# Performance work log

Hardware: AMD Instinct MI355X
Metric: run time of the kernel (lower is better)

## Reference

```python
import jax, jax.numpy as jnp
import numpy as np

B, S, D_IN, D_ATT = 8, 2048, 512, 512

def setup_inputs() -> dict:
    key = jax.random.key(0)
    ks = jax.random.split(key, 7)
    sc = 1.0 / np.sqrt(D_IN)
    return {
        "x": jax.random.normal(ks[0], (B, S, D_IN), dtype=jnp.float32),
        "Wq": jax.random.uniform(ks[1], (D_IN, D_ATT), jnp.float32, -sc, sc),
        "bq": jax.random.uniform(ks[2], (D_ATT,), jnp.float32, -sc, sc),
        "Wk": jax.random.uniform(ks[3], (D_IN, D_ATT), jnp.float32, -sc, sc),
        "bk": jax.random.uniform(ks[4], (D_ATT,), jnp.float32, -sc, sc),
        "Wv": jax.random.uniform(ks[5], (D_IN, D_ATT), jnp.float32, -sc, sc),
        "bv": jax.random.uniform(ks[6], (D_ATT,), jnp.float32, -sc, sc),
    }

def reference(x, Wq, bq, Wk, bk, Wv, bv):
    # Linear projections: [B, S, D_att]
    q = jnp.einsum("bsd,de->bse", x, Wq) + bq
    k = jnp.einsum("bsd,de->bse", x, Wk) + bk
    v = jnp.einsum("bsd,de->bse", x, Wv) + bv
    # Full scores matrix [B, S, S]; note: NO 1/sqrt(d) scaling in original.
    scores = jnp.einsum("bqe,bke->bqk", q, k)
    attn = jax.nn.softmax(scores, axis=-1)
    return jnp.einsum("bqk,bke->bqe", attn, v)
```

## Files before the change

### kernel.cpp

```cpp
#include <hip/hip_runtime.h>
#include <cstdint>
#include <cstddef>


#define SEQ 2048
#define DIM 512
#define NB 8
#define BSZ (NB * SEQ)
#define KT 64
#define NT (SEQ / KT)

typedef __attribute__((ext_vector_type(8))) _Float16 half8;
typedef __attribute__((ext_vector_type(4))) _Float16 half4;
typedef __attribute__((ext_vector_type(2))) __fp16 fp16x2;
typedef __attribute__((ext_vector_type(4))) float f32x4;
typedef __attribute__((ext_vector_type(16))) float f32x16;

__device__ __forceinline__ unsigned short f2h(float f) {
  _Float16 h = (_Float16)f;
  return __builtin_bit_cast(unsigned short, h);
}
__device__ __forceinline__ half8 ld_frag(const unsigned short* p) {
  return *(const half8*)(const void*)p;
}
__device__ __forceinline__ void gl_lds16(const unsigned short* g, unsigned short* l) {
  __builtin_amdgcn_global_load_lds(
      (__attribute__((address_space(1))) void*)g,
      (__attribute__((address_space(3))) void*)l, 16, 0, 0);
}
__device__ __forceinline__ void bar_vm0() {
  asm volatile("s_waitcnt vmcnt(0)\ns_barrier" ::: "memory");
}
__device__ __forceinline__ void bar_lgkm() {
  asm volatile("s_waitcnt lgkmcnt(0)\ns_barrier" ::: "memory");
}
__device__ __forceinline__ void bar_lgkm_vm0() {
  asm volatile("s_waitcnt lgkmcnt(0) vmcnt(0)\ns_barrier" ::: "memory");
}

__global__ __launch_bounds__(256) void cvt_x_kernel(
    const float* __restrict__ X, unsigned short* __restrict__ xh)
{
  size_t i0 = ((size_t)blockIdx.x * 256 + threadIdx.x) * 8;
  float4 a = *(const float4*)&X[i0];
  float4 b = *(const float4*)&X[i0 + 4];
  ushort4 o0; o0.x = f2h(a.x); o0.y = f2h(a.y); o0.z = f2h(a.z); o0.w = f2h(a.w);
  ushort4 o1; o1.x = f2h(b.x); o1.y = f2h(b.y); o1.z = f2h(b.z); o1.w = f2h(b.w);
  *(ushort4*)&xh[i0] = o0;
  *(ushort4*)&xh[i0 + 4] = o1;
}

__global__ __launch_bounds__(256) void cvt_w_kernel(
    const float* __restrict__ Wq, const float* __restrict__ Wk,
    const float* __restrict__ Wv, unsigned short* __restrict__ Wt)
{
  const int z = blockIdx.z;
  const float* W = (z == 0) ? Wq : (z == 1) ? Wk : Wv;
  unsigned short* out = Wt + (size_t)z * DIM * DIM;
  const int k0 = blockIdx.x * 64, n0 = blockIdx.y * 64;
  const int t = threadIdx.x;
  __shared__ unsigned short tl[64 * 72];
#pragma unroll
  for (int i = 0; i < 4; i++) {
    int f = t + 256 * i;
    int kr = f >> 4, c4 = (f & 15) * 4;
    float4 v = *(const float4*)&W[(size_t)(k0 + kr) * DIM + n0 + c4];
    tl[(c4 + 0) * 72 + kr] = f2h(v.x);
    tl[(c4 + 1) * 72 + kr] = f2h(v.y);
    tl[(c4 + 2) * 72 + kr] = f2h(v.z);
    tl[(c4 + 3) * 72 + kr] = f2h(v.w);
  }
  __syncthreads();
#pragma unroll
  for (int i = 0; i < 2; i++) {
    int f = t + 256 * i;
    int nr = f >> 3, k8 = (f & 7) * 8;
    *(uint4*)&out[(size_t)(n0 + nr) * DIM + k0 + k8] = *(const uint4*)&tl[nr * 72 + k8];
  }
}

__global__ __launch_bounds__(256) void proj_kernel(
    const unsigned short* __restrict__ xh, const unsigned short* __restrict__ Wt,
    const float* __restrict__ bq, const float* __restrict__ bk,
    const float* __restrict__ bv, unsigned short* __restrict__ outbase)
{
  const int z = blockIdx.z;
  const unsigned short* Wz = Wt + (size_t)z * DIM * DIM;
  const float* bias = (z == 0) ? bq : (z == 1) ? bk : bv;
  unsigned short* out = outbase + (size_t)z * BSZ * DIM;
  const int m0 = blockIdx.x * 128, n0 = blockIdx.y * 128;
  const int t = threadIdx.x, lane = t & 63, wave = t >> 6;
  const int wrow = (wave >> 1) * 64, wcol = (wave & 1) * 64;
  const int lr = lane & 15, lq = (lane >> 4) * 8;

  __shared__ unsigned short sm[128 * 132];
  unsigned short* As = sm;
  unsigned short* Bs = sm + 128 * 64;

  f32x4 acc[4][4];
  const f32x4 zero = {0.f, 0.f, 0.f, 0.f};
#pragma unroll
  for (int r = 0; r < 4; r++)
#pragma unroll
    for (int c = 0; c < 4; c++) acc[r][c] = zero;

  for (int k0 = 0; k0 < DIM; k0 += 64) {
    __syncthreads();
#pragma unroll
    for (int i = 0; i < 4; i++) {
      int f = t + 256 * i;
      int row = f >> 3, c8 = (f & 7) * 8;
      gl_lds16(&xh[(size_t)(m0 + row) * DIM + k0 + c8], &As[i * 2048 + wave * 512]);
      gl_lds16(&Wz[(size_t)(n0 + row) * DIM + k0 + c8], &Bs[i * 2048 + wave * 512]);
    }
    __syncthreads();
#pragma unroll
    for (int kk = 0; kk < 64; kk += 32) {
      half8 a[4], b[4];
#pragma unroll
      for (int r = 0; r < 4; r++) a[r] = ld_frag(&As[(wrow + 16 * r + lr) * 64 + kk + lq]);
#pragma unroll
      for (int c = 0; c < 4; c++) b[c] = ld_frag(&Bs[(wcol + 16 * c + lr) * 64 + kk + lq]);
#pragma unroll
      for (int r = 0; r < 4; r++)
#pragma unroll
        for (int c = 0; c < 4; c++)
          acc[r][c] = __builtin_amdgcn_mfma_f32_16x16x32_f16(a[r], b[c], acc[r][c], 0, 0, 0);
    }
  }
  __syncthreads();
#pragma unroll
  for (int c = 0; c < 4; c++) {
    float bb = bias[n0 + wcol + 16 * c + lr];
#pragma unroll
    for (int r = 0; r < 4; r++)
#pragma unroll
      for (int e = 0; e < 4; e++)
        sm[(wrow + 16 * r + (lane >> 4) * 4 + e) * 132 + wcol + 16 * c + lr] =
            f2h(acc[r][c][e] + bb);
  }
  __syncthreads();
#pragma unroll
  for (int i = 0; i < 8; i++) {
    int f = t + 256 * i;
    int row = f >> 4, c8 = (f & 15) * 8;
    *(uint4*)&out[(size_t)(m0 + row) * DIM + n0 + c8] = *(const uint4*)&sm[row * 132 + c8];
  }
}

__global__ __launch_bounds__(256) void vtrans_kernel(
    const unsigned short* __restrict__ vh, unsigned short* __restrict__ vt)
{
  const int b = blockIdx.z;
  const int s0 = blockIdx.x * 64, n0 = blockIdx.y * 64;
  const int t = threadIdx.x;
  __shared__ unsigned short tl[64 * 72];
#pragma unroll
  for (int i = 0; i < 2; i++) {
    int f = t + 256 * i;
    int sr = f >> 3, c8 = (f & 7) * 8;
    uint4 raw = *(const uint4*)&vh[((size_t)b * SEQ + s0 + sr) * DIM + n0 + c8];
    unsigned short u[8];
    *(uint4*)u = raw;
#pragma unroll
    for (int j = 0; j < 8; j++) tl[(c8 + j) * 72 + sr] = u[j];
  }
  __syncthreads();
#pragma unroll
  for (int i = 0; i < 2; i++) {
    int f = t + 256 * i;
    int nr = f >> 3, s8 = (f & 7) * 8;
    *(uint4*)&vt[((size_t)b * DIM + n0 + nr) * SEQ + s0 + s8] = *(const uint4*)&tl[nr * 72 + s8];
  }
}

#define PSTR 68
#define OSTR 516

__global__ __launch_bounds__(256, 1) void flash_kernel(
    const unsigned short* __restrict__ Qb, const unsigned short* __restrict__ Kb,
    const unsigned short* __restrict__ Vtb, float* __restrict__ Ob)
{
  const int zb = blockIdx.x & 7;
  const int q0 = (blockIdx.x >> 3) * 64;
  const unsigned short* Q = Qb + (size_t)zb * SEQ * DIM;
  const unsigned short* K = Kb + (size_t)zb * SEQ * DIM;
  const unsigned short* V = Vtb + (size_t)zb * DIM * SEQ;
  float* Out = Ob + (size_t)zb * SEQ * DIM;

  const int t = threadIdx.x, lane = t & 63, wave = t >> 6;
  const int l31 = lane & 31, hi = lane >> 5;
  const int kh = wave & 1, rh = wave >> 1;
  const int lr = lane & 15, lq4 = lane >> 4;
  const float L2E = 1.4426950408889634f;

  __shared__ unsigned short lds[70664];
  unsigned short* Qbuf = lds;
  unsigned short* Kbuf = lds + 32768;
  unsigned short* Pbuf = lds + 65536;
  float* mpart = (float*)(lds + 65536 + 64 * PSTR);
  float* lpart = mpart + 128;
  float* abuf = lpart + 128;
  float* lrun = abuf + 64;
  unsigned int* fbuf = (unsigned int*)(lrun + 64);

  if (t < 64) lrun[t] = 0.f;

  int koff[16];
#pragma unroll
  for (int i = 0; i < 16; i++) {
    int f = t + 256 * i;
    int row = f >> 6, c = f & 63;
    koff[i] = row * DIM + (c ^ (row & 7)) * 8;
  }

#pragma unroll
  for (int i = 0; i < 16; i++)
    gl_lds16(&Q[(size_t)q0 * DIM + koff[i]], &Qbuf[i * 2048 + wave * 512]);
#pragma unroll
  for (int i = 0; i < 16; i++)
    gl_lds16(&K[koff[i]], &Kbuf[i * 2048 + wave * 512]);

  f32x4 acc[32];
  const f32x4 zero = {0.f, 0.f, 0.f, 0.f};
#pragma unroll
  for (int ob = 0; ob < 32; ob++) acc[ob] = zero;
  float m_run = -__builtin_inff();

  const int keyrow = kh * 32 + l31, ksw = keyrow & 7;
  const int qrow = rh * 32 + l31, qsw = qrow & 7;
  const unsigned short* Kc = Kbuf + keyrow * 512;
  const unsigned short* Qc = Qbuf + qrow * 512;

  for (int kt = 0; kt < NT; kt++) {
    bar_vm0();

    const unsigned short* Vb = V + (size_t)(wave * 128 + lr) * SEQ + kt * KT + lq4 * 8;
    half8 vfA[8];
#pragma unroll
    for (int dc = 0; dc < 4; dc++)
#pragma unroll
      for (int ks = 0; ks < 2; ks++)
        vfA[dc * 2 + ks] = ld_frag(Vb + (size_t)dc * 16 * SEQ + ks * 32);

    f32x16 s0 = {0.f, 0.f, 0.f, 0.f, 0.f, 0.f, 0.f, 0.f,
                 0.f, 0.f, 0.f, 0.f, 0.f, 0.f, 0.f, 0.f};
    f32x16 s1 = s0;
    __builtin_amdgcn_s_setprio(1);
#pragma unroll
    for (int j = 0; j < 16; j++) {
      half8 kf0 = ld_frag(&Kc[((2 * j + hi) ^ ksw) << 3]);
      half8 qv0 = ld_frag(&Qc[((2 * j + hi) ^ qsw) << 3]);
      half8 kf1 = ld_frag(&Kc[((2 * (j + 16) + hi) ^ ksw) << 3]);
      half8 qv1 = ld_frag(&Qc[((2 * (j + 16) + hi) ^ qsw) << 3]);
      s0 = __builtin_amdgcn_mfma_f32_32x32x16_f16(kf0, qv0, s0, 0, 0, 0);
      s1 = __builtin_amdgcn_mfma_f32_32x32x16_f16(kf1, qv1, s1, 0, 0, 0);
    }
    __builtin_amdgcn_s_setprio(0);
    f32x16 sacc = s0 + s1;

    float mx = sacc[0];
#pragma unroll
    for (int i2 = 1; i2 < 16; i2++) mx = fmaxf(mx, sacc[i2]);
    mx = fmaxf(mx, __shfl_xor(mx, 32, 64));
    if (lane < 32) mpart[kh * 64 + rh * 32 + lane] = mx;
    bar_lgkm();

    if (kt + 1 < NT) {
      const unsigned short* Kt = K + (size_t)(kt + 1) * KT * DIM;
#pragma unroll
      for (int i = 0; i < 16; i++)
        gl_lds16(&Kt[koff[i]], &Kbuf[i * 2048 + wave * 512]);
    }
    half8 vfB[8];
#pragma unroll
    for (int dc = 0; dc < 4; dc++)
#pragma unroll
      for (int ks = 0; ks < 2; ks++)
        vfB[dc * 2 + ks] = ld_frag(Vb + (size_t)(dc + 4) * 16 * SEQ + ks * 32);

    float mo = mpart[(kh ^ 1) * 64 + rh * 32 + l31];
    float mxc = fmaxf(mx, mo);
    bool keep = (mxc - m_run <= 8.0f);
    float mnew = keep ? m_run : mxc;
    float alpha = keep ? 1.0f : exp2f((m_run - mnew) * L2E);
    m_run = mnew;
    if (kh == 0 && lane < 32) abuf[rh * 32 + lane] = alpha;
    unsigned long long ball = __ballot(keep);
    if (lane == 0) fbuf[wave] = (ball == ~0ull) ? 1u : 0u;

    float psum = 0.f;
#pragma unroll
    for (int w2 = 0; w2 < 4; w2++) {
      float p0 = exp2f((sacc[4 * w2 + 0] - mnew) * L2E);
      float p1 = exp2f((sacc[4 * w2 + 1] - mnew) * L2E);
      float p2 = exp2f((sacc[4 * w2 + 2] - mnew) * L2E);
      float p3 = exp2f((sacc[4 * w2 + 3] - mnew) * L2E);
      psum += (p0 + p1) + (p2 + p3);
      fp16x2 pa = __builtin_amdgcn_cvt_pkrtz(p0, p1);
      fp16x2 pb = __builtin_amdgcn_cvt_pkrtz(p2, p3);
      unsigned long long both =
          ((unsigned long long)__builtin_bit_cast(unsigned int, pb) << 32) |
          __builtin_bit_cast(unsigned int, pa);
      *(unsigned long long*)&Pbuf[qrow * PSTR + kh * 32 + w2 * 8 + 4 * hi] = both;
    }
    psum += __shfl_xor(psum, 32, 64);
    if (lane < 32) lpart[kh * 64 + rh * 32 + lane] = psum;
    bar_lgkm();
    if (kh == 0 && lane < 32) {
      int r = rh * 32 + lane;
      lrun[r] = alpha * lrun[r] + lpart[r] + lpart[64 + r];
    }

    if (!(fbuf[0] & fbuf[1] & fbuf[2] & fbuf[3])) {
#pragma unroll
      for (int rg = 0; rg < 4; rg++)
#pragma unroll
        for (int e = 0; e < 4; e++) {
          float a = abuf[rg * 16 + lq4 * 4 + e];
#pragma unroll
          for (int dc = 0; dc < 8; dc++) acc[rg * 8 + dc][e] *= a;
        }
    }

    half8 pf[4][2];
#pragma unroll
    for (int rg = 0; rg < 4; rg++)
#pragma unroll
      for (int ks = 0; ks < 2; ks++) {
        const unsigned short* pp = &Pbuf[(rg * 16 + lr) * PSTR + ks * 32 + lq4 * 8];
        half4 lo = *(const half4*)(const void*)pp;
        half4 h2 = *(const half4*)(const void*)(pp + 4);
        half8 v;
#pragma unroll
        for (int q = 0; q < 4; q++) { v[q] = lo[q]; v[4 + q] = h2[q]; }
        pf[rg][ks] = v;
      }
    __builtin_amdgcn_s_setprio(1);
#pragma unroll
    for (int dc = 0; dc < 4; dc++)
#pragma unroll
      for (int rg = 0; rg < 4; rg++) {
        acc[rg * 8 + dc] =
            __builtin_amdgcn_mfma_f32_16x16x32_f16(pf[rg][0], vfA[dc * 2 + 0],
                                                   acc[rg * 8 + dc], 0, 0, 0);
        acc[rg * 8 + dc] =
            __builtin_amdgcn_mfma_f32_16x16x32_f16(pf[rg][1], vfA[dc * 2 + 1],
                                                   acc[rg * 8 + dc], 0, 0, 0);
      }
#pragma unroll
    for (int dc = 4; dc < 8; dc++)
#pragma unroll
      for (int rg = 0; rg < 4; rg++) {
        acc[rg * 8 + dc] =
            __builtin_amdgcn_mfma_f32_16x16x32_f16(pf[rg][0], vfB[(dc - 4) * 2 + 0],
                                                   acc[rg * 8 + dc], 0, 0, 0);
        acc[rg * 8 + dc] =
            __builtin_amdgcn_mfma_f32_16x16x32_f16(pf[rg][1], vfB[(dc - 4) * 2 + 1],
                                                   acc[rg * 8 + dc], 0, 0, 0);
      }
    __builtin_amdgcn_s_setprio(0);
  }

  bar_lgkm_vm0();

  float linv[4][4];
#pragma unroll
  for (int rg = 0; rg < 4; rg++)
#pragma unroll
    for (int e = 0; e < 4; e++) linv[rg][e] = 1.0f / lrun[rg * 16 + lq4 * 4 + e];

  float* Obuf = (float*)lds;
#pragma unroll
  for (int h = 0; h < 2; h++) {
    __syncthreads();
#pragma unroll
    for (int r2 = 0; r2 < 2; r2++) {
      int rg = h * 2 + r2;
#pragma unroll
      for (int e = 0; e < 4; e++) {
        int rowh = r2 * 16 + lq4 * 4 + e;
#pragma unroll
        for (int dc = 0; dc < 8; dc++)
          Obuf[rowh * OSTR + wave * 128 + dc * 16 + lr] = acc[rg * 8 + dc][e] * linv[rg][e];
      }
    }
    __syncthreads();
#pragma unroll
    for (int i = 0; i < 16; i++) {
      int f = t + 256 * i;
      int rowh = f >> 7, c4 = (f & 127) * 4;
      *(float4*)&Out[(size_t)(q0 + h * 32 + rowh) * DIM + c4] =
          *(const float4*)&Obuf[rowh * OSTR + c4];
    }
  }
}

extern "C" void kernel_launch(void* const* d_in, const int* in_sizes, int n_in,
                              void* d_out, int out_size, void* d_ws, size_t ws_size,
                              hipStream_t stream)
{
  const float* X  = (const float*)d_in[0];
  const float* Wq = (const float*)d_in[1];
  const float* bq = (const float*)d_in[2];
  const float* Wk = (const float*)d_in[3];
  const float* bk = (const float*)d_in[4];
  const float* Wv = (const float*)d_in[5];
  const float* bv = (const float*)d_in[6];
  float* Out = (float*)d_out;

  char* ws = (char*)d_ws;
  const size_t MB = 1u << 20;
  unsigned short* qh = (unsigned short*)(ws);
  unsigned short* kh = (unsigned short*)(ws + 16 * MB);
  unsigned short* vh = (unsigned short*)(ws + 32 * MB);
  unsigned short* vt = (unsigned short*)(ws + 48 * MB);
  unsigned short* xh = (unsigned short*)(ws + 48 * MB);
  unsigned short* Wt = (unsigned short*)(ws + 64 * MB);

  cvt_x_kernel<<<dim3(BSZ * DIM / 2048), 256, 0, stream>>>(X, xh);
  cvt_w_kernel<<<dim3(8, 8, 3), 256, 0, stream>>>(Wq, Wk, Wv, Wt);
  proj_kernel<<<dim3(BSZ / 128, DIM / 128, 3), 256, 0, stream>>>(
      xh, Wt, bq, bk, bv, qh);
  vtrans_kernel<<<dim3(SEQ / 64, DIM / 64, NB), 256, 0, stream>>>(vh, vt);
  flash_kernel<<<dim3(NB * SEQ / 64), 256, 0, stream>>>(qh, kh, vt, Out);
}
```

Baseline: 293.2 us.

## Halve flash tile to 32 query rows and 32 keys for two blocks per CU

Shrinks the flash attention block from 64 query rows by 64 keys to 32 by 32. The QK step switches from 32x32 MFMA to 16x16 MFMA, and the accumulators, LDS usage and grid size change to match, so two blocks fit per CU and the grid doubles. The aim is to hide latency through higher occupancy and more blocks. In exchange, each block reuses loaded K/V across fewer queries, doubling global K/V traffic, and the loop runs twice as many iterations with their barriers and softmax overhead.

```diff
diff --git a/kernel.cpp b/kernel.cpp
--- a/kernel.cpp
+++ b/kernel.cpp
@@ -7,14 +7,13 @@
 #define DIM 512
 #define NB 8
 #define BSZ (NB * SEQ)
-#define KT 64
+#define KT 32
 #define NT (SEQ / KT)
+#define QROWS 32
 
 typedef __attribute__((ext_vector_type(8))) _Float16 half8;
-typedef __attribute__((ext_vector_type(4))) _Float16 half4;
 typedef __attribute__((ext_vector_type(2))) __fp16 fp16x2;
 typedef __attribute__((ext_vector_type(4))) float f32x4;
-typedef __attribute__((ext_vector_type(16))) float f32x16;
 
 __device__ __forceinline__ unsigned short f2h(float f) {
   _Float16 h = (_Float16)f;
@@ -174,61 +173,60 @@
   }
 }
 
-#define PSTR 68
+#define PSTR 40
 #define OSTR 516
 
-__global__ __launch_bounds__(256, 1) void flash_kernel(
+__global__ __launch_bounds__(256, 2) void flash_kernel(
     const unsigned short* __restrict__ Qb, const unsigned short* __restrict__ Kb,
     const unsigned short* __restrict__ Vtb, float* __restrict__ Ob)
 {
   const int zb = blockIdx.x & 7;
-  const int q0 = (blockIdx.x >> 3) * 64;
+  const int q0 = (blockIdx.x >> 3) * QROWS;
   const unsigned short* Q = Qb + (size_t)zb * SEQ * DIM;
   const unsigned short* K = Kb + (size_t)zb * SEQ * DIM;
   const unsigned short* V = Vtb + (size_t)zb * DIM * SEQ;
   float* Out = Ob + (size_t)zb * SEQ * DIM;
 
   const int t = threadIdx.x, lane = t & 63, wave = t >> 6;
-  const int l31 = lane & 31, hi = lane >> 5;
-  const int kh = wave & 1, rh = wave >> 1;
+  const int kq = wave & 1, rq = wave >> 1;
   const int lr = lane & 15, lq4 = lane >> 4;
   const float L2E = 1.4426950408889634f;
 
-  __shared__ unsigned short lds[70664];
+  __shared__ unsigned short lds[34448];
   unsigned short* Qbuf = lds;
-  unsigned short* Kbuf = lds + 32768;
-  unsigned short* Pbuf = lds + 65536;
-  float* mpart = (float*)(lds + 65536 + 64 * PSTR);
-  float* lpart = mpart + 128;
-  float* abuf = lpart + 128;
-  float* lrun = abuf + 64;
-  unsigned int* fbuf = (unsigned int*)(lrun + 64);
-
-  if (t < 64) lrun[t] = 0.f;
-
-  int koff[16];
-#pragma unroll
-  for (int i = 0; i < 16; i++) {
+  unsigned short* Kbuf = lds + 16384;
+  unsigned short* Pbuf = lds + 32768;
+  float* mpart = (float*)(lds + 34048);
+  float* lpart = (float*)(lds + 34176);
+  float* abuf  = (float*)(lds + 34304);
+  float* lrun  = (float*)(lds + 34368);
+  unsigned int* fbuf = (unsigned int*)(lds + 34432);
+
+  if (t < 32) lrun[t] = 0.f;
+
+  int koff[8];
+#pragma unroll
+  for (int i = 0; i < 8; i++) {
     int f = t + 256 * i;
     int row = f >> 6, c = f & 63;
     koff[i] = row * DIM + (c ^ (row & 7)) * 8;
   }
 
 #pragma unroll
-  for (int i = 0; i < 16; i++)
+  for (int i = 0; i < 8; i++)
     gl_lds16(&Q[(size_t)q0 * DIM + koff[i]], &Qbuf[i * 2048 + wave * 512]);
 #pragma unroll
-  for (int i = 0; i < 16; i++)
+  for (int i = 0; i < 8; i++)
     gl_lds16(&K[koff[i]], &Kbuf[i * 2048 + wave * 512]);
 
-  f32x4 acc[32];
+  f32x4 acc[16];
   const f32x4 zero = {0.f, 0.f, 0.f, 0.f};
 #pragma unroll
-  for (int ob = 0; ob < 32; ob++) acc[ob] = zero;
+  for (int ob = 0; ob < 16; ob++) acc[ob] = zero;
   float m_run = -__builtin_inff();
 
-  const int keyrow = kh * 32 + l31, ksw = keyrow & 7;
-  const int qrow = rh * 32 + l31, qsw = qrow & 7;
+  const int keyrow = kq * 16 + lr, ksw = keyrow & 7;
+  const int qrow = rq * 16 + lr, qsw = qrow & 7;
   const unsigned short* Kc = Kbuf + keyrow * 512;
   const unsigned short* Qc = Qbuf + qrow * 512;
 
@@ -236,85 +234,73 @@
     bar_vm0();
 
     const unsigned short* Vb = V + (size_t)(wave * 128 + lr) * SEQ + kt * KT + lq4 * 8;
-    half8 vfA[8];
-#pragma unroll
-    for (int dc = 0; dc < 4; dc++)
-#pragma unroll
-      for (int ks = 0; ks < 2; ks++)
-        vfA[dc * 2 + ks] = ld_frag(Vb + (size_t)dc * 16 * SEQ + ks * 32);
-
-    f32x16 s0 = {0.f, 0.f, 0.f, 0.f, 0.f, 0.f, 0.f, 0.f,
-                 0.f, 0.f, 0.f, 0.f, 0.f, 0.f, 0.f, 0.f};
-    f32x16 s1 = s0;
+    half8 vf[8];
+#pragma unroll
+    for (int dc = 0; dc < 8; dc++)
+      vf[dc] = ld_frag(Vb + (size_t)dc * 16 * SEQ);
+
+    f32x4 s0 = zero, s1 = zero;
     __builtin_amdgcn_s_setprio(1);
 #pragma unroll
-    for (int j = 0; j < 16; j++) {
-      half8 kf0 = ld_frag(&Kc[((2 * j + hi) ^ ksw) << 3]);
-      half8 qv0 = ld_frag(&Qc[((2 * j + hi) ^ qsw) << 3]);
-      half8 kf1 = ld_frag(&Kc[((2 * (j + 16) + hi) ^ ksw) << 3]);
-      half8 qv1 = ld_frag(&Qc[((2 * (j + 16) + hi) ^ qsw) << 3]);
-      s0 = __builtin_amdgcn_mfma_f32_32x32x16_f16(kf0, qv0, s0, 0, 0, 0);
-      s1 = __builtin_amdgcn_mfma_f32_32x32x16_f16(kf1, qv1, s1, 0, 0, 0);
+    for (int j = 0; j < 8; j++) {
+      half8 kf0 = ld_frag(&Kc[(((4 * j + lq4) ^ ksw) << 3)]);
+      half8 qv0 = ld_frag(&Qc[(((4 * j + lq4) ^ qsw) << 3)]);
+      half8 kf1 = ld_frag(&Kc[(((4 * (j + 8) + lq4) ^ ksw) << 3)]);
+      half8 qv1 = ld_frag(&Qc[(((4 * (j + 8) + lq4) ^ qsw) << 3)]);
+      s0 = __builtin_amdgcn_mfma_f32_16x16x32_f16(kf0, qv0, s0, 0, 0, 0);
+      s1 = __builtin_amdgcn_mfma_f32_16x16x32_f16(kf1, qv1, s1, 0, 0, 0);
     }
     __builtin_amdgcn_s_setprio(0);
-    f32x16 sacc = s0 + s1;
-
-    float mx = sacc[0];
-#pragma unroll
-    for (int i2 = 1; i2 < 16; i2++) mx = fmaxf(mx, sacc[i2]);
+    f32x4 sacc = s0 + s1;
+
+    float mx = fmaxf(fmaxf(sacc[0], sacc[1]), fmaxf(sacc[2], sacc[3]));
+    mx = fmaxf(mx, __shfl_xor(mx, 16, 64));
     mx = fmaxf(mx, __shfl_xor(mx, 32, 64));
-    if (lane < 32) mpart[kh * 64 + rh * 32 + lane] = mx;
+    if (lane < 16) mpart[kq * 32 + rq * 16 + lane] = mx;
     bar_lgkm();
 
     if (kt + 1 < NT) {
       const unsigned short* Kt = K + (size_t)(kt + 1) * KT * DIM;
 #pragma unroll
-      for (int i = 0; i < 16; i++)
+      for (int i = 0; i < 8; i++)
         gl_lds16(&Kt[koff[i]], &Kbuf[i * 2048 + wave * 512]);
     }
-    half8 vfB[8];
-#pragma unroll
-    for (int dc = 0; dc < 4; dc++)
-#pragma unroll
-      for (int ks = 0; ks < 2; ks++)
-        vfB[dc * 2 + ks] = ld_frag(Vb + (size_t)(dc + 4) * 16 * SEQ + ks * 32);
-
-    float mo = mpart[(kh ^ 1) * 64 + rh * 32 + l31];
+
+    float mo = mpart[(kq ^ 1) * 32 + rq * 16 + lr];
     float mxc = fmaxf(mx, mo);
     bool keep = (mxc - m_run <= 8.0f);
     float mnew = keep ? m_run : mxc;
     float alpha = keep ? 1.0f : exp2f((m_run - mnew) * L2E);
     m_run = mnew;
-    if (kh == 0 && lane < 32) abuf[rh * 32 + lane] = alpha;
+    if (kq == 0 && lane < 16) abuf[rq * 16 + lane] = alpha;
     unsigned long long ball = __ballot(keep);
     if (lane == 0) fbuf[wave] = (ball == ~0ull) ? 1u : 0u;
 
-    float psum = 0.f;
-#pragma unroll
-    for (int w2 = 0; w2 < 4; w2++) {
-      float p0 = exp2f((sacc[4 * w2 + 0] - mnew) * L2E);
-      float p1 = exp2f((sacc[4 * w2 + 1] - mnew) * L2E);
-      float p2 = exp2f((sacc[4 * w2 + 2] - mnew) * L2E);
-      float p3 = exp2f((sacc[4 * w2 + 3] - mnew) * L2E);
-      psum += (p0 + p1) + (p2 + p3);
+    float p0 = exp2f((sacc[0] - mnew) * L2E);
+    float p1 = exp2f((sacc[1] - mnew) * L2E);
+    float p2 = exp2f((sacc[2] - mnew) * L2E);
+    float p3 = exp2f((sacc[3] - mnew) * L2E);
+    float psum = (p0 + p1) + (p2 + p3);
+    {
       fp16x2 pa = __builtin_amdgcn_cvt_pkrtz(p0, p1);
       fp16x2 pb = __builtin_amdgcn_cvt_pkrtz(p2, p3);
       unsigned long long both =
           ((unsigned long long)__builtin_bit_cast(unsigned int, pb) << 32) |
           __builtin_bit_cast(unsigned int, pa);
-      *(unsigned long long*)&Pbuf[qrow * PSTR + kh * 32 + w2 * 8 + 4 * hi] = both;
-    }
+      *(unsigned long long*)&Pbuf[qrow * PSTR + kq * 16 + lq4 * 4] = both;
+    }
+    psum += __shfl_xor(psum, 16, 64);
     psum += __shfl_xor(psum, 32, 64);
-    if (lane < 32) lpart[kh * 64 + rh * 32 + lane] = psum;
+    if (lane < 16) lpart[kq * 32 + rq * 16 + lane] = psum;
     bar_lgkm();
-    if (kh == 0 && lane < 32) {
-      int r = rh * 32 + lane;
-      lrun[r] = alpha * lrun[r] + lpart[r] + lpart[64 + r];
+    if (kq == 0 && lane < 16) {
+      int r = rq * 16 + lane;
+      lrun[r] = alpha * lrun[r] + lpart[r] + lpart[32 + r];
     }
 
     if (!(fbuf[0] & fbuf[1] & fbuf[2] & fbuf[3])) {
 #pragma unroll
-      for (int rg = 0; rg < 4; rg++)
+      for (int rg = 0; rg < 2; rg++)
 #pragma unroll
         for (int e = 0; e < 4; e++) {
           float a = abuf[rg * 16 + lq4 * 4 + e];
@@ -323,76 +309,44 @@
         }
     }
 
-    half8 pf[4][2];
-#pragma unroll
-    for (int rg = 0; rg < 4; rg++)
-#pragma unroll
-      for (int ks = 0; ks < 2; ks++) {
-        const unsigned short* pp = &Pbuf[(rg * 16 + lr) * PSTR + ks * 32 + lq4 * 8];
-        half4 lo = *(const half4*)(const void*)pp;
-        half4 h2 = *(const half4*)(const void*)(pp + 4);
-        half8 v;
-#pragma unroll
-        for (int q = 0; q < 4; q++) { v[q] = lo[q]; v[4 + q] = h2[q]; }
-        pf[rg][ks] = v;
-      }
+    half8 pf[2];
+#pragma unroll
+    for (int rg = 0; rg < 2; rg++)
+      pf[rg] = ld_frag(&Pbuf[(rg * 16 + lr) * PSTR + lq4 * 8]);
     __builtin_amdgcn_s_setprio(1);
 #pragma unroll
-    for (int dc = 0; dc < 4; dc++)
-#pragma unroll
-      for (int rg = 0; rg < 4; rg++) {
+    for (int dc = 0; dc < 8; dc++)
+#pragma unroll
+      for (int rg = 0; rg < 2; rg++)
         acc[rg * 8 + dc] =
-            __builtin_amdgcn_mfma_f32_16x16x32_f16(pf[rg][0], vfA[dc * 2 + 0],
-                                                   acc[rg * 8 + dc], 0, 0, 0);
-        acc[rg * 8 + dc] =
-            __builtin_amdgcn_mfma_f32_16x16x32_f16(pf[rg][1], vfA[dc * 2 + 1],
-                                                   acc[rg * 8 + dc], 0, 0, 0);
-      }
-#pragma unroll
-    for (int dc = 4; dc < 8; dc++)
-#pragma unroll
-      for (int rg = 0; rg < 4; rg++) {
-        acc[rg * 8 + dc] =
-            __builtin_amdgcn_mfma_f32_16x16x32_f16(pf[rg][0], vfB[(dc - 4) * 2 + 0],
-                                                   acc[rg * 8 + dc], 0, 0, 0);
-        acc[rg * 8 + dc] =
-            __builtin_amdgcn_mfma_f32_16x16x32_f16(pf[rg][1], vfB[(dc - 4) * 2 + 1],
-                                                   acc[rg * 8 + dc], 0, 0, 0);
-      }
+            __builtin_amdgcn_mfma_f32_16x16x32_f16(pf[rg], vf[dc], acc[rg * 8 + dc], 0, 0, 0);
     __builtin_amdgcn_s_setprio(0);
   }
 
   bar_lgkm_vm0();
 
-  float linv[4][4];
-#pragma unroll
-  for (int rg = 0; rg < 4; rg++)
+  float linv[2][4];
+#pragma unroll
+  for (int rg = 0; rg < 2; rg++)
 #pragma unroll
     for (int e = 0; e < 4; e++) linv[rg][e] = 1.0f / lrun[rg * 16 + lq4 * 4 + e];
 
   float* Obuf = (float*)lds;
 #pragma unroll
-  for (int h = 0; h < 2; h++) {
-    __syncthreads();
-#pragma unroll
-    for (int r2 = 0; r2 < 2; r2++) {
-      int rg = h * 2 + r2;
-#pragma unroll
-      for (int e = 0; e < 4; e++) {
-        int rowh = r2 * 16 + lq4 * 4 + e;
-#pragma unroll
-        for (int dc = 0; dc < 8; dc++)
-          Obuf[rowh * OSTR + wave * 128 + dc * 16 + lr] = acc[rg * 8 + dc][e] * linv[rg][e];
-      }
-    }
-    __syncthreads();
-#pragma unroll
-    for (int i = 0; i < 16; i++) {
-      int f = t + 256 * i;
-      int rowh = f >> 7, c4 = (f & 127) * 4;
-      *(float4*)&Out[(size_t)(q0 + h * 32 + rowh) * DIM + c4] =
-          *(const float4*)&Obuf[rowh * OSTR + c4];
-    }
+  for (int rg = 0; rg < 2; rg++)
+#pragma unroll
+    for (int e = 0; e < 4; e++) {
+      int row = rg * 16 + lq4 * 4 + e;
+#pragma unroll
+      for (int dc = 0; dc < 8; dc++)
+        Obuf[row * OSTR + wave * 128 + dc * 16 + lr] = acc[rg * 8 + dc][e] * linv[rg][e];
+    }
+  __syncthreads();
+#pragma unroll
+  for (int i = 0; i < 16; i++) {
+    int f = t + 256 * i;
+    int row = f >> 7, c4 = (f & 127) * 4;
+    *(float4*)&Out[(size_t)(q0 + row) * DIM + c4] = *(const float4*)&Obuf[row * OSTR + c4];
   }
 }
 
@@ -423,5 +377,5 @@
   proj_kernel<<<dim3(BSZ / 128, DIM / 128, 3), 256, 0, stream>>>(
       xh, Wt, bq, bk, bv, qh);
   vtrans_kernel<<<dim3(SEQ / 64, DIM / 64, NB), 256, 0, stream>>>(vh, vt);
-  flash_kernel<<<dim3(NB * SEQ / 64), 256, 0, stream>>>(qh, kh, vt, Out);
-}
+  flash_kernel<<<dim3(NB * SEQ / QROWS), 256, 0, stream>>>(qh, kh, vt, Out);
+}
```

Result: slower. 334.3 us (+14.0%).

## Halve flash query tile, keep Q in registers, split QK over head-dim halves

Applied to the files above, without the earlier changes.

Flash attention now processes 32 query rows per block instead of 64, so twice as many blocks launch, and launch bounds allow two blocks per CU. Q fragments are loaded once into registers. The QK^T dot product is split across wave pairs over halves of the head dimension, and partial scores are reduced through an LDS exchange buffer. This lowers LDS and register use per block to raise occupancy and latency hiding. In exchange, each query row now drives twice the K/V reads from L2, there is an extra LDS reduction and barrier, and only half the waves run the softmax.

```diff
diff --git a/kernel.cpp b/kernel.cpp
--- a/kernel.cpp
+++ b/kernel.cpp
@@ -9,6 +9,7 @@
 #define BSZ (NB * SEQ)
 #define KT 64
 #define NT (SEQ / KT)
+#define QROWS 32
 
 typedef __attribute__((ext_vector_type(8))) _Float16 half8;
 typedef __attribute__((ext_vector_type(4))) _Float16 half4;
@@ -176,13 +177,14 @@
 
 #define PSTR 68
 #define OSTR 516
-
-__global__ __launch_bounds__(256, 1) void flash_kernel(
+#define XSTR 18
+
+__global__ __launch_bounds__(256, 2) void flash_kernel(
     const unsigned short* __restrict__ Qb, const unsigned short* __restrict__ Kb,
     const unsigned short* __restrict__ Vtb, float* __restrict__ Ob)
 {
   const int zb = blockIdx.x & 7;
-  const int q0 = (blockIdx.x >> 3) * 64;
+  const int q0 = (blockIdx.x >> 3) * QROWS;
   const unsigned short* Q = Qb + (size_t)zb * SEQ * DIM;
   const unsigned short* K = Kb + (size_t)zb * SEQ * DIM;
   const unsigned short* V = Vtb + (size_t)zb * DIM * SEQ;
@@ -190,47 +192,55 @@
 
   const int t = threadIdx.x, lane = t & 63, wave = t >> 6;
   const int l31 = lane & 31, hi = lane >> 5;
-  const int kh = wave & 1, rh = wave >> 1;
+  const int kh = wave & 1, sh = wave >> 1;
   const int lr = lane & 15, lq4 = lane >> 4;
   const float L2E = 1.4426950408889634f;
 
-  __shared__ unsigned short lds[70664];
-  unsigned short* Qbuf = lds;
-  unsigned short* Kbuf = lds + 32768;
-  unsigned short* Pbuf = lds + 65536;
-  float* mpart = (float*)(lds + 65536 + 64 * PSTR);
-  float* lpart = mpart + 128;
-  float* abuf = lpart + 128;
-  float* lrun = abuf + 64;
-  unsigned int* fbuf = (unsigned int*)(lrun + 64);
-
-  if (t < 64) lrun[t] = 0.f;
-
-  int koff[16];
-#pragma unroll
-  for (int i = 0; i < 16; i++) {
+  __shared__ unsigned short lds[39944];
+  unsigned short* Kbuf = lds;
+  unsigned short* Pbuf = lds + 32768;
+  float* xbuf = (float*)(lds + 34944);
+  float* mpart = (float*)(lds + 39552);
+  float* lpart = mpart + 64;
+  float* abuf  = lpart + 64;
+  float* lrun  = abuf + 32;
+  unsigned int* fbuf = (unsigned int*)(lrun + 32);
+
+  if (t < 32) lrun[t] = 0.f;
+
+  int koff[8];
+#pragma unroll
+  for (int i = 0; i < 8; i++) {
     int f = t + 256 * i;
     int row = f >> 6, c = f & 63;
     koff[i] = row * DIM + (c ^ (row & 7)) * 8;
   }
 
 #pragma unroll
+  for (int i = 0; i < 8; i++)
+    gl_lds16(&Q[(size_t)q0 * DIM + koff[i]], &Kbuf[i * 2048 + wave * 512]);
+  bar_lgkm_vm0();
+  half8 qf[16];
+  {
+    const int qrow = l31, qsw = qrow & 7;
+#pragma unroll
+    for (int j = 0; j < 16; j++)
+      qf[j] = ld_frag(&Kbuf[qrow * 512 + (((32 * sh + 2 * j + hi) ^ qsw) << 3)]);
+  }
+  __syncthreads();
+#pragma unroll
   for (int i = 0; i < 16; i++)
-    gl_lds16(&Q[(size_t)q0 * DIM + koff[i]], &Qbuf[i * 2048 + wave * 512]);
-#pragma unroll
-  for (int i = 0; i < 16; i++)
-    gl_lds16(&K[koff[i]], &Kbuf[i * 2048 + wave * 512]);
-
-  f32x4 acc[32];
+    gl_lds16(&K[koff[i & 7] + (i >> 3) * 32 * DIM], &Kbuf[i * 2048 + wave * 512]);
+
+  f32x4 acc[16];
   const f32x4 zero = {0.f, 0.f, 0.f, 0.f};
 #pragma unroll
-  for (int ob = 0; ob < 32; ob++) acc[ob] = zero;
+  for (int ob = 0; ob < 16; ob++) acc[ob] = zero;
   float m_run = -__builtin_inff();
 
   const int keyrow = kh * 32 + l31, ksw = keyrow & 7;
-  const int qrow = rh * 32 + l31, qsw = qrow & 7;
   const unsigned short* Kc = Kbuf + keyrow * 512;
-  const unsigned short* Qc = Qbuf + qrow * 512;
+  float* xme = &xbuf[(size_t)kh * 64 * XSTR + lane * XSTR];
 
   for (int kt = 0; kt < NT; kt++) {
     bar_vm0();
@@ -243,78 +253,93 @@
       for (int ks = 0; ks < 2; ks++)
         vfA[dc * 2 + ks] = ld_frag(Vb + (size_t)dc * 16 * SEQ + ks * 32);
 
-    f32x16 s0 = {0.f, 0.f, 0.f, 0.f, 0.f, 0.f, 0.f, 0.f,
-                 0.f, 0.f, 0.f, 0.f, 0.f, 0.f, 0.f, 0.f};
-    f32x16 s1 = s0;
+    f32x16 s0c = {0.f, 0.f, 0.f, 0.f, 0.f, 0.f, 0.f, 0.f,
+                  0.f, 0.f, 0.f, 0.f, 0.f, 0.f, 0.f, 0.f};
+    f32x16 s1c = s0c;
     __builtin_amdgcn_s_setprio(1);
 #pragma unroll
-    for (int j = 0; j < 16; j++) {
-      half8 kf0 = ld_frag(&Kc[((2 * j + hi) ^ ksw) << 3]);
-      half8 qv0 = ld_frag(&Qc[((2 * j + hi) ^ qsw) << 3]);
-      half8 kf1 = ld_frag(&Kc[((2 * (j + 16) + hi) ^ ksw) << 3]);
-      half8 qv1 = ld_frag(&Qc[((2 * (j + 16) + hi) ^ qsw) << 3]);
-      s0 = __builtin_amdgcn_mfma_f32_32x32x16_f16(kf0, qv0, s0, 0, 0, 0);
-      s1 = __builtin_amdgcn_mfma_f32_32x32x16_f16(kf1, qv1, s1, 0, 0, 0);
+    for (int j = 0; j < 8; j++) {
+      half8 kf0 = ld_frag(&Kc[((32 * sh + 2 * j + hi) ^ ksw) << 3]);
+      half8 kf1 = ld_frag(&Kc[((32 * sh + 2 * (j + 8) + hi) ^ ksw) << 3]);
+      s0c = __builtin_amdgcn_mfma_f32_32x32x16_f16(kf0, qf[j], s0c, 0, 0, 0);
+      s1c = __builtin_amdgcn_mfma_f32_32x32x16_f16(kf1, qf[j + 8], s1c, 0, 0, 0);
     }
     __builtin_amdgcn_s_setprio(0);
-    f32x16 sacc = s0 + s1;
-
-    float mx = sacc[0];
-#pragma unroll
-    for (int i2 = 1; i2 < 16; i2++) mx = fmaxf(mx, sacc[i2]);
-    mx = fmaxf(mx, __shfl_xor(mx, 32, 64));
-    if (lane < 32) mpart[kh * 64 + rh * 32 + lane] = mx;
+    f32x16 sacc = s0c + s1c;
+
+    if (sh == 1) {
+#pragma unroll
+      for (int q = 0; q < 8; q++) {
+        float2 v2; v2.x = sacc[2 * q]; v2.y = sacc[2 * q + 1];
+        *(float2*)&xme[2 * q] = v2;
+      }
+    }
     bar_lgkm();
 
+    half8 vfB[8];
+#pragma unroll
+    for (int dc = 0; dc < 4; dc++)
+#pragma unroll
+      for (int ks = 0; ks < 2; ks++)
+        vfB[dc * 2 + ks] = ld_frag(Vb + (size_t)(dc + 4) * 16 * SEQ + ks * 32);
     if (kt + 1 < NT) {
       const unsigned short* Kt = K + (size_t)(kt + 1) * KT * DIM;
 #pragma unroll
       for (int i = 0; i < 16; i++)
-        gl_lds16(&Kt[koff[i]], &Kbuf[i * 2048 + wave * 512]);
-    }
-    half8 vfB[8];
-#pragma unroll
-    for (int dc = 0; dc < 4; dc++)
-#pragma unroll
-      for (int ks = 0; ks < 2; ks++)
-        vfB[dc * 2 + ks] = ld_frag(Vb + (size_t)(dc + 4) * 16 * SEQ + ks * 32);
-
-    float mo = mpart[(kh ^ 1) * 64 + rh * 32 + l31];
-    float mxc = fmaxf(mx, mo);
-    bool keep = (mxc - m_run <= 8.0f);
-    float mnew = keep ? m_run : mxc;
-    float alpha = keep ? 1.0f : exp2f((m_run - mnew) * L2E);
-    m_run = mnew;
-    if (kh == 0 && lane < 32) abuf[rh * 32 + lane] = alpha;
-    unsigned long long ball = __ballot(keep);
-    if (lane == 0) fbuf[wave] = (ball == ~0ull) ? 1u : 0u;
-
-    float psum = 0.f;
-#pragma unroll
-    for (int w2 = 0; w2 < 4; w2++) {
-      float p0 = exp2f((sacc[4 * w2 + 0] - mnew) * L2E);
-      float p1 = exp2f((sacc[4 * w2 + 1] - mnew) * L2E);
-      float p2 = exp2f((sacc[4 * w2 + 2] - mnew) * L2E);
-      float p3 = exp2f((sacc[4 * w2 + 3] - mnew) * L2E);
-      psum += (p0 + p1) + (p2 + p3);
-      fp16x2 pa = __builtin_amdgcn_cvt_pkrtz(p0, p1);
-      fp16x2 pb = __builtin_amdgcn_cvt_pkrtz(p2, p3);
-      unsigned long long both =
-          ((unsigned long long)__builtin_bit_cast(unsigned int, pb) << 32) |
-          __builtin_bit_cast(unsigned int, pa);
-      *(unsigned long long*)&Pbuf[qrow * PSTR + kh * 32 + w2 * 8 + 4 * hi] = both;
-    }
-    psum += __shfl_xor(psum, 32, 64);
-    if (lane < 32) lpart[kh * 64 + rh * 32 + lane] = psum;
+        gl_lds16(&Kt[koff[i & 7] + (i >> 3) * 32 * DIM], &Kbuf[i * 2048 + wave * 512]);
+    }
+
+    if (sh == 0) {
+#pragma unroll
+      for (int q = 0; q < 8; q++) {
+        float2 v2 = *(const float2*)&xme[2 * q];
+        sacc[2 * q] += v2.x;
+        sacc[2 * q + 1] += v2.y;
+      }
+      float mx = sacc[0];
+#pragma unroll
+      for (int i2 = 1; i2 < 16; i2++) mx = fmaxf(mx, sacc[i2]);
+      mx = fmaxf(mx, __shfl_xor(mx, 32, 64));
+      if (lane < 32) mpart[kh * 32 + lane] = mx;
+    }
     bar_lgkm();
-    if (kh == 0 && lane < 32) {
-      int r = rh * 32 + lane;
-      lrun[r] = alpha * lrun[r] + lpart[r] + lpart[64 + r];
-    }
-
-    if (!(fbuf[0] & fbuf[1] & fbuf[2] & fbuf[3])) {
-#pragma unroll
-      for (int rg = 0; rg < 4; rg++)
+
+    if (sh == 0) {
+      float mxc = fmaxf(mpart[lane & 31], mpart[32 + (lane & 31)]);
+      bool keep = (mxc - m_run <= 8.0f);
+      float mnew = keep ? m_run : mxc;
+      float alpha = keep ? 1.0f : exp2f((m_run - mnew) * L2E);
+      m_run = mnew;
+      if (kh == 0 && lane < 32) abuf[lane] = alpha;
+      unsigned long long ball = __ballot(keep);
+      if (lane == 0) fbuf[kh] = (ball == ~0ull) ? 1u : 0u;
+      float psum = 0.f;
+#pragma unroll
+      for (int w2 = 0; w2 < 4; w2++) {
+        float p0 = exp2f((sacc[4 * w2 + 0] - mnew) * L2E);
+        float p1 = exp2f((sacc[4 * w2 + 1] - mnew) * L2E);
+        float p2 = exp2f((sacc[4 * w2 + 2] - mnew) * L2E);
+        float p3 = exp2f((sacc[4 * w2 + 3] - mnew) * L2E);
+        psum += (p0 + p1) + (p2 + p3);
+        fp16x2 pa = __builtin_amdgcn_cvt_pkrtz(p0, p1);
+        fp16x2 pb = __builtin_amdgcn_cvt_pkrtz(p2, p3);
+        unsigned long long both =
+            ((unsigned long long)__builtin_bit_cast(unsigned int, pb) << 32) |
+            __builtin_bit_cast(unsigned int, pa);
+        *(unsigned long long*)&Pbuf[l31 * PSTR + kh * 32 + w2 * 8 + 4 * hi] = both;
+      }
+      psum += __shfl_xor(psum, 32, 64);
+      if (lane < 32) lpart[kh * 32 + lane] = psum;
+    }
+    bar_lgkm();
+    if (sh == 0 && kh == 0 && lane < 32) {
+      float a = abuf[lane];
+      lrun[lane] = a * lrun[lane] + lpart[lane] + lpart[32 + lane];
+    }
+
+    if (!(fbuf[0] & fbuf[1])) {
+#pragma unroll
+      for (int rg = 0; rg < 2; rg++)
 #pragma unroll
         for (int e = 0; e < 4; e++) {
           float a = abuf[rg * 16 + lq4 * 4 + e];
@@ -323,9 +348,9 @@
         }
     }
 
-    half8 pf[4][2];
-#pragma unroll
-    for (int rg = 0; rg < 4; rg++)
+    half8 pf[2][2];
+#pragma unroll
+    for (int rg = 0; rg < 2; rg++)
 #pragma unroll
       for (int ks = 0; ks < 2; ks++) {
         const unsigned short* pp = &Pbuf[(rg * 16 + lr) * PSTR + ks * 32 + lq4 * 8];
@@ -340,7 +365,7 @@
 #pragma unroll
     for (int dc = 0; dc < 4; dc++)
 #pragma unroll
-      for (int rg = 0; rg < 4; rg++) {
+      for (int rg = 0; rg < 2; rg++) {
         acc[rg * 8 + dc] =
             __builtin_amdgcn_mfma_f32_16x16x32_f16(pf[rg][0], vfA[dc * 2 + 0],
                                                    acc[rg * 8 + dc], 0, 0, 0);
@@ -351,7 +376,7 @@
 #pragma unroll
     for (int dc = 4; dc < 8; dc++)
 #pragma unroll
-      for (int rg = 0; rg < 4; rg++) {
+      for (int rg = 0; rg < 2; rg++) {
         acc[rg * 8 + dc] =
             __builtin_amdgcn_mfma_f32_16x16x32_f16(pf[rg][0], vfB[(dc - 4) * 2 + 0],
                                                    acc[rg * 8 + dc], 0, 0, 0);
@@ -364,35 +389,29 @@
 
   bar_lgkm_vm0();
 
-  float linv[4][4];
-#pragma unroll
-  for (int rg = 0; rg < 4; rg++)
+  float linv[2][4];
+#pragma unroll
+  for (int rg = 0; rg < 2; rg++)
 #pragma unroll
     for (int e = 0; e < 4; e++) linv[rg][e] = 1.0f / lrun[rg * 16 + lq4 * 4 + e];
 
   float* Obuf = (float*)lds;
-#pragma unroll
-  for (int h = 0; h < 2; h++) {
-    __syncthreads();
-#pragma unroll
-    for (int r2 = 0; r2 < 2; r2++) {
-      int rg = h * 2 + r2;
-#pragma unroll
-      for (int e = 0; e < 4; e++) {
-        int rowh = r2 * 16 + lq4 * 4 + e;
-#pragma unroll
-        for (int dc = 0; dc < 8; dc++)
-          Obuf[rowh * OSTR + wave * 128 + dc * 16 + lr] = acc[rg * 8 + dc][e] * linv[rg][e];
-      }
-    }
-    __syncthreads();
-#pragma unroll
-    for (int i = 0; i < 16; i++) {
-      int f = t + 256 * i;
-      int rowh = f >> 7, c4 = (f & 127) * 4;
-      *(float4*)&Out[(size_t)(q0 + h * 32 + rowh) * DIM + c4] =
-          *(const float4*)&Obuf[rowh * OSTR + c4];
-    }
+  __syncthreads();
+#pragma unroll
+  for (int rg = 0; rg < 2; rg++)
+#pragma unroll
+    for (int e = 0; e < 4; e++) {
+      int row = rg * 16 + lq4 * 4 + e;
+#pragma unroll
+      for (int dc = 0; dc < 8; dc++)
+        Obuf[row * OSTR + wave * 128 + dc * 16 + lr] = acc[rg * 8 + dc][e] * linv[rg][e];
+    }
+  __syncthreads();
+#pragma unroll
+  for (int i = 0; i < 16; i++) {
+    int f = t + 256 * i;
+    int row = f >> 7, c4 = (f & 127) * 4;
+    *(float4*)&Out[(size_t)(q0 + row) * DIM + c4] = *(const float4*)&Obuf[row * OSTR + c4];
   }
 }
 
@@ -423,5 +442,5 @@
   proj_kernel<<<dim3(BSZ / 128, DIM / 128, 3), 256, 0, stream>>>(
       xh, Wt, bq, bk, bv, qh);
   vtrans_kernel<<<dim3(SEQ / 64, DIM / 64, NB), 256, 0, stream>>>(vh, vt);
-  flash_kernel<<<dim3(NB * SEQ / 64), 256, 0, stream>>>(qh, kh, vt, Out);
-}
+  flash_kernel<<<dim3(NB * SEQ / QROWS), 256, 0, stream>>>(qh, kh, vt, Out);
+}
```

Result: slower. 394.2 us (+34.5%).
